# Kernel tuning notes

Hardware: AMD Instinct MI355X
Metric: run time of the kernel (lower is better)

## Reference

```python
import jax, jax.numpy as jnp
import numpy as np

B, S, D = 2, 2048, 4096
H, KV, HD = 32, 8, 128          # query heads, kv heads, head_dim
N_REP = H // KV                 # GQA groups = 4
ROPE_THETA = 1000000.0


def setup_inputs() -> dict:
    key = jax.random.key(0)
    ks = jax.random.split(key, 8)
    s = 0.02
    return {
        "hidden_states": jax.random.normal(ks[0], (B, S, D), jnp.float32),
        "position_ids": jnp.broadcast_to(jnp.arange(S, dtype=jnp.int32)[None, :], (B, S)),
        "wq": jax.random.normal(ks[1], (D, H * HD), jnp.float32) * s,
        "bq": jax.random.normal(ks[2], (H * HD,), jnp.float32) * s,
        "wk": jax.random.normal(ks[3], (D, KV * HD), jnp.float32) * s,
        "bk": jax.random.normal(ks[4], (KV * HD,), jnp.float32) * s,
        "wv": jax.random.normal(ks[5], (D, KV * HD), jnp.float32) * s,
        "bv": jax.random.normal(ks[6], (KV * HD,), jnp.float32) * s,
        "wo": jax.random.normal(ks[7], (H * HD, D), jnp.float32) * s,
    }


def _rope_cos_sin(position_ids, head_dim, theta):
    pos = position_ids.astype(jnp.float32)
    dim = head_dim // 2
    freqs = 1.0 / theta ** (jnp.arange(0, dim, dtype=jnp.float32) / dim)
    t = pos[..., None] * freqs[None, None, :]          # [B,S,dim]
    return jnp.cos(t)[..., None, :], jnp.sin(t)[..., None, :]  # [B,S,1,dim]


def _apply_rope(x, cos, sin):
    half = x.shape[-1] // 2
    x1, x2 = x[..., :half], x[..., half:]
    return jnp.concatenate([x1 * cos - x2 * sin, x1 * sin + x2 * cos], axis=-1)


def reference(hidden_states, position_ids, wq, bq, wk, bk, wv, bv, wo):
    q = (hidden_states @ wq + bq).reshape(B, S, H, HD)
    k = (hidden_states @ wk + bk).reshape(B, S, KV, HD)
    v = (hidden_states @ wv + bv).reshape(B, S, KV, HD)

    cos, sin = _rope_cos_sin(position_ids, HD, ROPE_THETA)
    q = _apply_rope(q, cos, sin)
    k = _apply_rope(k, cos, sin)

    # GQA: physically expand KV heads (adjacent repeats, matches repeat_kv)
    k = jnp.repeat(k, N_REP, axis=2)   # [B,S,H,HD]
    v = jnp.repeat(v, N_REP, axis=2)

    # causal bias (attention_mask defaults to all-ones, so only causal matters)
    neg = jnp.finfo(jnp.float32).min
    causal = jnp.tril(jnp.ones((S, S), dtype=bool))
    bias = jnp.where(causal, 0.0, neg).astype(jnp.float32)  # [S,S]

    scale = 1.0 / jnp.sqrt(jnp.float32(HD))
    scores = jnp.einsum("bqhd,bkhd->bhqk", q * scale, k) + bias[None, None]
    attn = jax.nn.softmax(scores, axis=-1)                  # [B,H,S,S]
    out = jnp.einsum("bhqk,bkhd->bqhd", attn, v)
    out = out.reshape(B, S, H * HD)
    return out @ wo
```

## Files before the change

kernel.cpp:

```cpp
#include <hip/hip_runtime.h>
#include <hip/hip_bf16.h>
#include <math.h>


typedef __bf16 bf16;
typedef __attribute__((ext_vector_type(8))) __bf16 bf16x8;
typedef __attribute__((ext_vector_type(4))) float f32x4;

__device__ __forceinline__ void glds16(const void* g, void* l) {
    __builtin_amdgcn_global_load_lds(
        (const __attribute__((address_space(1))) void*)g,
        (__attribute__((address_space(3))) void*)l, 16, 0, 0);
}

__device__ __forceinline__ unsigned cvt_pk_bf16(float lo, float hi) {
    unsigned r;
    asm("v_cvt_pk_bf16_f32 %0, %1, %2" : "=v"(r) : "v"(lo), "v"(hi));
    return r;
}

__global__ __launch_bounds__(256) void convert_kernel(
    const float* __restrict__ in, bf16* __restrict__ out)
{
    const size_t i0 = ((size_t)blockIdx.x * 256 + threadIdx.x) * 8;
    const float4 a = *(const float4*)(in + i0);
    const float4 b = *(const float4*)(in + i0 + 4);
    bf16x8 p;
    p[0] = (bf16)a.x; p[1] = (bf16)a.y; p[2] = (bf16)a.z; p[3] = (bf16)a.w;
    p[4] = (bf16)b.x; p[5] = (bf16)b.y; p[6] = (bf16)b.z; p[7] = (bf16)b.w;
    *(bf16x8*)(out + i0) = p;
}

__global__ __launch_bounds__(256) void transpose_conv_kernel(
    const float* __restrict__ in, bf16* __restrict__ out, int N)
{
    __shared__ bf16 tile[32 * 68];
    const int n0 = blockIdx.x * 32, k0 = blockIdx.y * 64;
    const int t = threadIdx.x;
    const int nn = t & 31, kk0 = (t >> 5) * 8;
#pragma unroll
    for (int j = 0; j < 8; ++j)
        tile[nn * 68 + kk0 + j] = (bf16)in[(size_t)(k0 + kk0 + j) * N + n0 + nn];
    __syncthreads();
    const int n2 = t >> 3, c = (t & 7) * 8;
    *(bf16x8*)(out + (size_t)(n0 + n2) * 4096 + k0 + c) = *(const bf16x8*)(&tile[n2 * 68 + c]);
}

template <int EPI, int AF32>
__global__ __launch_bounds__(256) void gemm_kernel(
    const float* __restrict__ A_f32, const bf16* __restrict__ A_bf16,
    const bf16* __restrict__ BqT, const bf16* __restrict__ BkT, const bf16* __restrict__ BvT,
    const float* __restrict__ b_q, const float* __restrict__ b_k, const float* __restrict__ b_v,
    bf16* __restrict__ q_out, bf16* __restrict__ kv_k, bf16* __restrict__ kv_v,
    float* __restrict__ f_out)
{
    constexpr int LDA = AF32 ? 34 : 32;
    __shared__ bf16 As[128 * LDA];
    __shared__ bf16 Bs[128 * 32];

    const int nt = blockIdx.x, mt = blockIdx.y;
    const int tid = threadIdx.x;
    const int wave = tid >> 6, lane = tid & 63;
    const int l15 = lane & 15, quad = lane >> 4;
    const int wm = (wave >> 1) * 64, wn = (wave & 1) * 64;

    const bf16* BT;
    const float* bias = nullptr;
    int sel = 0, ncol0;
    if (EPI == 0) {
        if (nt < 32)      { BT = BqT; bias = b_q; sel = 0; ncol0 = nt * 128; }
        else if (nt < 40) { BT = BkT; bias = b_k; sel = 1; ncol0 = (nt - 32) * 128; }
        else              { BT = BvT; bias = b_v; sel = 2; ncol0 = (nt - 40) * 128; }
    } else {
        BT = BqT; ncol0 = nt * 128;
    }
    const int row0 = mt * 128;

    const f32x4 vzero = {0.f, 0.f, 0.f, 0.f};
    f32x4 acc[4][4];
#pragma unroll
    for (int mi = 0; mi < 4; ++mi)
#pragma unroll
        for (int ni = 0; ni < 4; ++ni) acc[mi][ni] = vzero;

    const int a_row = tid >> 1, a_seg = (tid & 1) * 16;
    const int g_row = lane >> 2, g_seg = (lane & 3) * 8;

    for (int k0 = 0; k0 < 4096; k0 += 32) {
        if (AF32) {
            const float4* src = (const float4*)(A_f32 + (size_t)(row0 + a_row) * 4096 + k0 + a_seg);
            float4 f0 = src[0], f1 = src[1], f2 = src[2], f3 = src[3];
            bf16x8 p0, p1;
            p0[0] = (bf16)f0.x; p0[1] = (bf16)f0.y; p0[2] = (bf16)f0.z; p0[3] = (bf16)f0.w;
            p0[4] = (bf16)f1.x; p0[5] = (bf16)f1.y; p0[6] = (bf16)f1.z; p0[7] = (bf16)f1.w;
            p1[0] = (bf16)f2.x; p1[1] = (bf16)f2.y; p1[2] = (bf16)f2.z; p1[3] = (bf16)f2.w;
            p1[4] = (bf16)f3.x; p1[5] = (bf16)f3.y; p1[6] = (bf16)f3.z; p1[7] = (bf16)f3.w;
            *(bf16x8*)(&As[a_row * LDA + a_seg]) = p0;
            *(bf16x8*)(&As[a_row * LDA + a_seg + 8]) = p1;
        } else {
#pragma unroll
            for (int c = 0; c < 2; ++c)
                glds16(A_bf16 + (size_t)(row0 + wave * 32 + c * 16 + g_row) * 4096 + k0 + g_seg,
                       &As[(wave * 32 + c * 16) * 32]);
        }
#pragma unroll
        for (int c = 0; c < 2; ++c)
            glds16(BT + (size_t)(ncol0 + wave * 32 + c * 16 + g_row) * 4096 + k0 + g_seg,
                   &Bs[(wave * 32 + c * 16) * 32]);
        __syncthreads();

        bf16x8 af[4], bfv[4];
#pragma unroll
        for (int mi = 0; mi < 4; ++mi)
            af[mi] = *(const bf16x8*)(&As[(wm + mi * 16 + l15) * LDA + quad * 8]);
#pragma unroll
        for (int ni = 0; ni < 4; ++ni)
            bfv[ni] = *(const bf16x8*)(&Bs[(wn + ni * 16 + l15) * 32 + quad * 8]);
#pragma unroll
        for (int mi = 0; mi < 4; ++mi)
#pragma unroll
            for (int ni = 0; ni < 4; ++ni)
                acc[mi][ni] = __builtin_amdgcn_mfma_f32_16x16x32_bf16(af[mi], bfv[ni], acc[mi][ni], 0, 0, 0);
        __syncthreads();
    }

#pragma unroll
    for (int mi = 0; mi < 4; ++mi)
#pragma unroll
        for (int ni = 0; ni < 4; ++ni)
#pragma unroll
            for (int i = 0; i < 4; ++i) {
                const int gr = row0 + wm + mi * 16 + quad * 4 + i;
                const int gc = ncol0 + wn + ni * 16 + l15;
                float vv = acc[mi][ni][i];
                if (EPI == 1) {
                    f_out[(size_t)gr * 4096 + gc] = vv;
                } else {
                    vv += bias[gc];
                    if (sel == 0) {
                        q_out[(size_t)gr * 4096 + gc] = (bf16)vv;
                    } else {
                        bf16* dst = (sel == 1) ? kv_k : kv_v;
                        dst[(size_t)((gr >> 11) * 8 + (gc >> 7)) * 262144 +
                            (size_t)(gr & 2047) * 128 + (gc & 127)] = (bf16)vv;
                    }
                }
            }
}

__global__ __launch_bounds__(256) void rope_q_kernel(
    bf16* __restrict__ q, const int* __restrict__ pos_ids)
{
    const int idx = blockIdx.x * 256 + threadIdx.x;
    const int d = idx & 63, h = (idx >> 6) & 31, tok = idx >> 11;
    const float posv = (float)pos_ids[tok];
    const float fr = exp2f((float)d * (-19.931568569324174f / 64.f));
    float sn, cs;
    sincosf(posv * fr, &sn, &cs);
    bf16* xp = q + (size_t)tok * 4096 + h * 128 + d;
    const float x1 = (float)xp[0], x2 = (float)xp[64];
    const float scale = 0.08838834764831845f;
    xp[0]  = (bf16)((x1 * cs - x2 * sn) * scale);
    xp[64] = (bf16)((x1 * sn + x2 * cs) * scale);
}

__global__ __launch_bounds__(256) void rope_k_kernel(
    bf16* __restrict__ k, const int* __restrict__ pos_ids)
{
    const int idx = blockIdx.x * 256 + threadIdx.x;
    const int d = idx & 63, s = (idx >> 6) & 2047, bk = idx >> 17;
    const int b = bk >> 3;
    const float posv = (float)pos_ids[b * 2048 + s];
    const float fr = exp2f((float)d * (-19.931568569324174f / 64.f));
    float sn, cs;
    sincosf(posv * fr, &sn, &cs);
    bf16* xp = k + ((size_t)bk * 2048 + s) * 128 + d;
    const float x1 = (float)xp[0], x2 = (float)xp[64];
    xp[0]  = (bf16)(x1 * cs - x2 * sn);
    xp[64] = (bf16)(x1 * sn + x2 * cs);
}

__global__ __launch_bounds__(256) void attn_kernel(
    const bf16* __restrict__ q, const bf16* __restrict__ k,
    const bf16* __restrict__ v, bf16* __restrict__ o)
{
    __shared__ bf16 Ksl[64 * 136];
    __shared__ bf16 Vsl[128 * 72];
    __shared__ bf16 Psl[4 * 16 * 68];

    const int pair = blockIdx.x & 7;
    const int h  = (blockIdx.x >> 3) & 31;
    const int b  = blockIdx.x >> 8;
    const int kvh = h >> 2;
    const int tid = threadIdx.x;
    const int wave = tid >> 6, lane = tid & 63;
    const int l15 = lane & 15, quad = lane >> 4;

    const bf16* kbase = k + (size_t)(b * 8 + kvh) * 2048 * 128;
    const bf16* vbase = v + (size_t)(b * 8 + kvh) * 2048 * 128;

    const int kr = tid >> 2, ksg = (tid & 3) * 32;
    const f32x4 vzero = {0.f, 0.f, 0.f, 0.f};

#pragma unroll 1
    for (int phase = 0; phase < 2; ++phase) {
        const int qt = phase ? (15 - pair) : pair;
        const int qbase = qt * 128 + wave * 32;

        bf16x8 qf[2][4];
#pragma unroll
        for (int mi = 0; mi < 2; ++mi) {
            const bf16* qrow = q + ((size_t)(b * 2048 + qbase + mi * 16 + l15) * 32 + h) * 128;
#pragma unroll
            for (int kb = 0; kb < 4; ++kb)
                qf[mi][kb] = *(const bf16x8*)(qrow + kb * 32 + quad * 8);
        }

        f32x4 acc_o[2][8];
#pragma unroll
        for (int mi = 0; mi < 2; ++mi)
#pragma unroll
            for (int i = 0; i < 8; ++i) acc_o[mi][i] = vzero;
        float m_i[2] = {-INFINITY, -INFINITY};
        float l_i[2] = {0.f, 0.f};

        const int nT = 2 * qt + 2;
        for (int t = 0; t < nT; ++t) {
            const int kv0 = t * 64;
            {
                const bf16x8* ks = (const bf16x8*)(kbase + (size_t)(kv0 + kr) * 128 + ksg);
                bf16x8* kd = (bf16x8*)(&Ksl[kr * 136 + ksg]);
                kd[0] = ks[0]; kd[1] = ks[1]; kd[2] = ks[2]; kd[3] = ks[3];
            }
            {
                const bf16x8* vs = (const bf16x8*)(vbase + (size_t)(kv0 + lane) * 128 + wave * 32);
                bf16x8 w0 = vs[0], w1 = vs[1], w2 = vs[2], w3 = vs[3];
#pragma unroll
                for (int i = 0; i < 8; ++i) {
                    Vsl[(wave * 32 + i)      * 72 + lane] = w0[i];
                    Vsl[(wave * 32 + 8 + i)  * 72 + lane] = w1[i];
                    Vsl[(wave * 32 + 16 + i) * 72 + lane] = w2[i];
                    Vsl[(wave * 32 + 24 + i) * 72 + lane] = w3[i];
                }
            }
            __syncthreads();

            if (kv0 <= qbase + 31) {
                f32x4 sacc[2][4];
#pragma unroll
                for (int mi = 0; mi < 2; ++mi)
#pragma unroll
                    for (int nt = 0; nt < 4; ++nt) sacc[mi][nt] = vzero;
                __builtin_amdgcn_s_setprio(1);
#pragma unroll
                for (int nt = 0; nt < 4; ++nt)
#pragma unroll
                    for (int kb = 0; kb < 4; ++kb) {
                        const bf16x8 kf = *(const bf16x8*)(&Ksl[(nt * 16 + l15) * 136 + kb * 32 + quad * 8]);
                        sacc[0][nt] = __builtin_amdgcn_mfma_f32_16x16x32_bf16(kf, qf[0][kb], sacc[0][nt], 0, 0, 0);
                        sacc[1][nt] = __builtin_amdgcn_mfma_f32_16x16x32_bf16(kf, qf[1][kb], sacc[1][nt], 0, 0, 0);
                    }
                __builtin_amdgcn_s_setprio(0);

                bf16x8 pf[2][2];
#pragma unroll
                for (int mi = 0; mi < 2; ++mi) {
                    const int rb = qbase + mi * 16;
                    if (kv0 + 63 > rb) {
#pragma unroll
                        for (int nt = 0; nt < 4; ++nt) {
                            const int kvr = kv0 + nt * 16 + quad * 4;
#pragma unroll
                            for (int i = 0; i < 4; ++i)
                                if (kvr + i > rb + l15) sacc[mi][nt][i] = -INFINITY;
                        }
                    }
                    float tm;
                    {
                        f32x4 m4;
#pragma unroll
                        for (int i = 0; i < 4; ++i)
                            m4[i] = fmaxf(fmaxf(sacc[mi][0][i], sacc[mi][1][i]),
                                          fmaxf(sacc[mi][2][i], sacc[mi][3][i]));
                        tm = fmaxf(fmaxf(m4[0], m4[1]), fmaxf(m4[2], m4[3]));
                        tm = fmaxf(tm, __shfl_xor(tm, 16, 64));
                        tm = fmaxf(tm, __shfl_xor(tm, 32, 64));
                    }
                    if (!__all(tm - m_i[mi] <= 8.f)) {
                        const float mnew = fmaxf(m_i[mi], tm);
                        const float alpha = __expf(m_i[mi] - mnew);
                        m_i[mi] = mnew;
                        l_i[mi] *= alpha;
                        float aw[4];
#pragma unroll
                        for (int i = 0; i < 4; ++i)
                            aw[i] = __shfl(alpha, quad * 4 + i, 16);
#pragma unroll
                        for (int dn = 0; dn < 8; ++dn)
#pragma unroll
                            for (int i = 0; i < 4; ++i) acc_o[mi][dn][i] *= aw[i];
                    }
                    float p[4][4];
                    float rs = 0.f;
#pragma unroll
                    for (int nt = 0; nt < 4; ++nt)
#pragma unroll
                        for (int i = 0; i < 4; ++i) {
                            p[nt][i] = __expf(sacc[mi][nt][i] - m_i[mi]);
                            rs += p[nt][i];
                        }
                    rs += __shfl_xor(rs, 16, 64);
                    rs += __shfl_xor(rs, 32, 64);
                    l_i[mi] += rs;
#pragma unroll
                    for (int nt = 0; nt < 4; ++nt) {
                        uint2 w;
                        w.x = cvt_pk_bf16(p[nt][0], p[nt][1]);
                        w.y = cvt_pk_bf16(p[nt][2], p[nt][3]);
                        *(uint2*)(&Psl[wave * 1088 + l15 * 68 + nt * 16 + quad * 4]) = w;
                    }
#pragma unroll
                    for (int k2 = 0; k2 < 2; ++k2)
                        pf[mi][k2] = *(const bf16x8*)(&Psl[wave * 1088 + l15 * 68 + k2 * 32 + quad * 8]);
                }

                __builtin_amdgcn_s_setprio(1);
#pragma unroll
                for (int dn = 0; dn < 8; ++dn)
#pragma unroll
                    for (int k2 = 0; k2 < 2; ++k2) {
                        const bf16x8 vf = *(const bf16x8*)(&Vsl[(dn * 16 + l15) * 72 + k2 * 32 + quad * 8]);
                        acc_o[0][dn] = __builtin_amdgcn_mfma_f32_16x16x32_bf16(pf[0][k2], vf, acc_o[0][dn], 0, 0, 0);
                        acc_o[1][dn] = __builtin_amdgcn_mfma_f32_16x16x32_bf16(pf[1][k2], vf, acc_o[1][dn], 0, 0, 0);
                    }
                __builtin_amdgcn_s_setprio(0);
            }
            __syncthreads();
        }

#pragma unroll
        for (int mi = 0; mi < 2; ++mi) {
            const float inv = 1.f / l_i[mi];
            float invw[4];
#pragma unroll
            for (int i = 0; i < 4; ++i)
                invw[i] = __shfl(inv, quad * 4 + i, 16);
#pragma unroll
            for (int dn = 0; dn < 8; ++dn)
#pragma unroll
                for (int i = 0; i < 4; ++i) {
                    const int s = qbase + mi * 16 + quad * 4 + i;
                    o[(((size_t)b * 2048 + s) * 32 + h) * 128 + dn * 16 + l15] =
                        (bf16)(acc_o[mi][dn][i] * invw[i]);
                }
        }
    }
}

extern "C" void kernel_launch(void* const* d_in, const int* in_sizes, int n_in,
                              void* d_out, int out_size, void* d_ws, size_t ws_size,
                              hipStream_t stream)
{
    (void)in_sizes; (void)n_in; (void)out_size;
    const float* hidden = (const float*)d_in[0];
    const int*   pos    = (const int*)d_in[1];
    const float* wq     = (const float*)d_in[2];
    const float* bq_    = (const float*)d_in[3];
    const float* wk     = (const float*)d_in[4];
    const float* bk_    = (const float*)d_in[5];
    const float* wv     = (const float*)d_in[6];
    const float* bv_    = (const float*)d_in[7];
    const float* wo     = (const float*)d_in[8];
    float* out = (float*)d_out;

    char* ws = (char*)d_ws;
    bf16* wqT   = (bf16*)(ws);
    bf16* wkT   = (bf16*)(ws + 33554432);
    bf16* wvT   = (bf16*)(ws + 41943040);
    bf16* q_pre = (bf16*)(ws + 50331648);
    bf16* k_t   = (bf16*)(ws + 83886080);
    bf16* v_t   = (bf16*)(ws + 92274688);
    bf16* hid_b = (bf16*)(ws + 100663296);
    bf16* attn_o = wqT;
    bf16* woT    = q_pre;
    const bool have_hid = (ws_size >= 134217728);

    transpose_conv_kernel<<<dim3(128, 64), 256, 0, stream>>>(wq, wqT, 4096);
    transpose_conv_kernel<<<dim3(32, 64), 256, 0, stream>>>(wk, wkT, 1024);
    transpose_conv_kernel<<<dim3(32, 64), 256, 0, stream>>>(wv, wvT, 1024);

    if (have_hid) {
        convert_kernel<<<8192, 256, 0, stream>>>(hidden, hid_b);
        gemm_kernel<0, 0><<<dim3(48, 32), 256, 0, stream>>>(
            nullptr, hid_b, wqT, wkT, wvT, bq_, bk_, bv_, q_pre, k_t, v_t, nullptr);
    } else {
        gemm_kernel<0, 1><<<dim3(48, 32), 256, 0, stream>>>(
            hidden, nullptr, wqT, wkT, wvT, bq_, bk_, bv_, q_pre, k_t, v_t, nullptr);
    }

    rope_q_kernel<<<32768, 256, 0, stream>>>(q_pre, pos);
    rope_k_kernel<<<8192, 256, 0, stream>>>(k_t, pos);

    attn_kernel<<<512, 256, 0, stream>>>(q_pre, k_t, v_t, attn_o);

    transpose_conv_kernel<<<dim3(128, 64), 256, 0, stream>>>(wo, woT, 4096);

    gemm_kernel<1, 0><<<dim3(32, 32), 256, 0, stream>>>(
        nullptr, attn_o, woT, nullptr, nullptr, nullptr, nullptr, nullptr,
        nullptr, nullptr, nullptr, out);
}
```

Measured before the change: 872.5 us.

## Add 256x256-tile 8-wave pipelined GEMM for QKV and output projections

Adds a new bf16 GEMM kernel that uses 256x256 output tiles with 512 threads and 128 KB of LDS. It double-buffers K slices with global_load_lds in a staged pipeline, uses XOR-swizzled LDS layouts and s_setprio around MFMA bursts, and remaps workgroups for cache locality. The kernel replaces the 128x128 GEMM for the QKV and output projections when the workspace holds the bf16 hidden buffer. The goal is more data reuse per tile and overlap of loads with MFMA work. The cost is lower occupancy and a smaller grid (384 and 256 blocks), which may leave CUs underused.

```diff
diff --git a/kernel.cpp b/kernel.cpp
--- a/kernel.cpp
+++ b/kernel.cpp
@@ -44,6 +44,173 @@
     __syncthreads();
     const int n2 = t >> 3, c = (t & 7) * 8;
     *(bf16x8*)(out + (size_t)(n0 + n2) * 4096 + k0 + c) = *(const bf16x8*)(&tile[n2 * 68 + c]);
+}
+
+#define G256_LDA(dst, bufv, mh)                                                 \
+    do {                                                                        \
+        _Pragma("unroll")                                                       \
+        for (int m_ = 0; m_ < 4; ++m_) {                                        \
+            const int rowh_ = (m_ * 2 + wr) * 16 + l15;                         \
+            const int colp_ = (quad * 8) ^ (((rowh_ >> 3) & 1) << 4);           \
+            const int bse_ = ((bufv) * 2 + (mh)) * 8192 + rowh_ * 32 + colp_;   \
+            dst[m_][0] = *(const bf16x8*)&Lds[bse_];                            \
+            dst[m_][1] = *(const bf16x8*)&Lds[bse_ + 4096];                     \
+        }                                                                       \
+    } while (0)
+
+#define G256_LDB(dst, bufv, nh)                                                 \
+    do {                                                                        \
+        _Pragma("unroll")                                                       \
+        for (int n_ = 0; n_ < 2; ++n_) {                                        \
+            const int rowh_ = (n_ * 4 + wc) * 16 + l15;                         \
+            const int colp_ = (quad * 8) ^ (((rowh_ >> 3) & 1) << 4);           \
+            const int bse_ = 32768 + ((bufv) * 2 + (nh)) * 8192 +               \
+                             rowh_ * 32 + colp_;                                \
+            dst[n_][0] = *(const bf16x8*)&Lds[bse_];                            \
+            dst[n_][1] = *(const bf16x8*)&Lds[bse_ + 4096];                     \
+        }                                                                       \
+    } while (0)
+
+#define G256_QUAD(av, bv, mh, nh)                                               \
+    do {                                                                        \
+        __builtin_amdgcn_s_setprio(1);                                          \
+        _Pragma("unroll")                                                       \
+        for (int m_ = 0; m_ < 4; ++m_)                                          \
+            _Pragma("unroll")                                                   \
+            for (int n_ = 0; n_ < 2; ++n_) {                                    \
+                acc[(mh) * 4 + m_][(nh) * 2 + n_] =                             \
+                    __builtin_amdgcn_mfma_f32_16x16x32_bf16(                    \
+                        av[m_][0], bv[n_][0], acc[(mh) * 4 + m_][(nh) * 2 + n_],\
+                        0, 0, 0);                                               \
+                acc[(mh) * 4 + m_][(nh) * 2 + n_] =                             \
+                    __builtin_amdgcn_mfma_f32_16x16x32_bf16(                    \
+                        av[m_][1], bv[n_][1], acc[(mh) * 4 + m_][(nh) * 2 + n_],\
+                        0, 0, 0);                                               \
+            }                                                                   \
+        __builtin_amdgcn_s_setprio(0);                                          \
+    } while (0)
+
+template <int EPI>
+__global__ __launch_bounds__(512) void gemm256_kernel(
+    const bf16* __restrict__ A,
+    const bf16* __restrict__ BqT, const bf16* __restrict__ BkT, const bf16* __restrict__ BvT,
+    const float* __restrict__ b_q, const float* __restrict__ b_k, const float* __restrict__ b_v,
+    bf16* __restrict__ q_out, bf16* __restrict__ kv_k, bf16* __restrict__ kv_v,
+    float* __restrict__ f_out, int nwg)
+{
+    __shared__ bf16 Lds[65536];
+
+    const int tid = threadIdx.x;
+    const int wv = tid >> 6, lane = tid & 63;
+    const int l15 = lane & 15, quad = lane >> 4;
+    const int wr = wv >> 2, wc = wv & 3;
+
+    const int bid = blockIdx.x;
+    const int swz = (bid & 7) * (nwg >> 3) + (bid >> 3);
+    const int mt = swz & 15, nt = swz >> 4;
+    const int row0 = mt * 256;
+
+    const bf16* BT;
+    const float* biasp = nullptr;
+    bf16* dstkv = nullptr;
+    int sel = 0, bcol0, ocol0 = nt * 256, lcol0 = 0;
+    if (EPI == 0) {
+        if (nt < 16)      { BT = BqT; bcol0 = nt * 256; biasp = b_q + nt * 256; sel = 0; }
+        else if (nt < 20) { BT = BkT; bcol0 = (nt - 16) * 256; biasp = b_k + (nt - 16) * 256;
+                            sel = 1; dstkv = kv_k; lcol0 = (nt - 16) * 256; }
+        else              { BT = BvT; bcol0 = (nt - 20) * 256; biasp = b_v + (nt - 20) * 256;
+                            sel = 2; dstkv = kv_v; lcol0 = (nt - 20) * 256; }
+    } else {
+        BT = BqT; bcol0 = nt * 256;
+    }
+
+    auto stage = [&](int n) {
+        if (n >= 256) return;
+        const int T = n >> 2, j = n & 3;
+        const int buf = T & 1;
+        const bool isA = (j == 0 || j == 3);
+        const int half = (j == 0) ? 0 : (j == 3) ? 1 : (j - 1);
+        const int k0 = T * 64;
+        const bf16* g = isA ? (A + (size_t)(row0 + half * 128) * 4096)
+                            : (BT + (size_t)(bcol0 + half * 128) * 4096);
+        bf16* lb = &Lds[(isA ? 0 : 32768) + (buf * 2 + half) * 8192];
+#pragma unroll
+        for (int jj = 0; jj < 2; ++jj) {
+            const int pc = (wv * 2 + jj) * 64 + lane;
+            const int kk = pc >> 9, rem = pc & 511;
+            const int row = rem >> 2, ccp = rem & 3;
+            const int ccl = ccp ^ ((row >> 2) & 2);
+            glds16(g + (size_t)row * 4096 + k0 + kk * 32 + ccl * 8,
+                   lb + (wv * 2 + jj) * 512);
+        }
+    };
+
+    const f32x4 vzero = {0.f, 0.f, 0.f, 0.f};
+    f32x4 acc[8][4];
+#pragma unroll
+    for (int mi = 0; mi < 8; ++mi)
+#pragma unroll
+        for (int ni = 0; ni < 4; ++ni) acc[mi][ni] = vzero;
+
+    bf16x8 a[4][2], b0[2][2], b1[2][2];
+
+    for (int n = 0; n < 7; ++n) stage(n);
+    asm volatile("s_waitcnt vmcnt(6)" ::: "memory");
+    __builtin_amdgcn_s_barrier();
+
+    for (int t = 0; t < 64; ++t) {
+        const int buf = t & 1;
+        const int nb = 4 * t;
+        G256_LDA(a, buf, 0);
+        G256_LDB(b0, buf, 0);
+        stage(nb + 7);
+        __builtin_amdgcn_s_barrier();
+        G256_QUAD(a, b0, 0, 0);
+        __builtin_amdgcn_s_barrier();
+        G256_LDB(b1, buf, 1);
+        stage(nb + 8);
+        __builtin_amdgcn_s_barrier();
+        G256_QUAD(a, b1, 0, 1);
+        __builtin_amdgcn_s_barrier();
+        G256_LDA(a, buf, 1);
+        stage(nb + 9);
+        __builtin_amdgcn_s_barrier();
+        G256_QUAD(a, b0, 1, 0);
+        __builtin_amdgcn_s_barrier();
+        stage(nb + 10);
+        __builtin_amdgcn_s_barrier();
+        G256_QUAD(a, b1, 1, 1);
+        if (t < 62)       asm volatile("s_waitcnt vmcnt(6)" ::: "memory");
+        else if (t == 62) asm volatile("s_waitcnt vmcnt(0)" ::: "memory");
+        __builtin_amdgcn_s_barrier();
+    }
+
+#pragma unroll
+    for (int mi = 0; mi < 8; ++mi) {
+        const int mtile = (mi >> 2) * 8 + (mi & 3) * 2 + wr;
+#pragma unroll
+        for (int ni = 0; ni < 4; ++ni) {
+            const int ntile = ni * 4 + wc;
+            const int gcl = ntile * 16 + l15;
+#pragma unroll
+            for (int i = 0; i < 4; ++i) {
+                const int gr = row0 + mtile * 16 + quad * 4 + i;
+                float vv = acc[mi][ni][i];
+                if (EPI == 1) {
+                    f_out[(size_t)gr * 4096 + ocol0 + gcl] = vv;
+                } else {
+                    vv += biasp[gcl];
+                    if (sel == 0) {
+                        q_out[(size_t)gr * 4096 + ocol0 + gcl] = (bf16)vv;
+                    } else {
+                        const int lc = lcol0 + gcl;
+                        dstkv[(size_t)((gr >> 11) * 8 + (lc >> 7)) * 262144 +
+                              (size_t)(gr & 2047) * 128 + (lc & 127)] = (bf16)vv;
+                    }
+                }
+            }
+        }
+    }
 }
 
 template <int EPI, int AF32>
@@ -391,8 +558,8 @@
 
     if (have_hid) {
         convert_kernel<<<8192, 256, 0, stream>>>(hidden, hid_b);
-        gemm_kernel<0, 0><<<dim3(48, 32), 256, 0, stream>>>(
-            nullptr, hid_b, wqT, wkT, wvT, bq_, bk_, bv_, q_pre, k_t, v_t, nullptr);
+        gemm256_kernel<0><<<384, 512, 0, stream>>>(
+            hid_b, wqT, wkT, wvT, bq_, bk_, bv_, q_pre, k_t, v_t, nullptr, 384);
     } else {
         gemm_kernel<0, 1><<<dim3(48, 32), 256, 0, stream>>>(
             hidden, nullptr, wqT, wkT, wvT, bq_, bk_, bv_, q_pre, k_t, v_t, nullptr);
@@ -405,7 +572,13 @@
 
     transpose_conv_kernel<<<dim3(128, 64), 256, 0, stream>>>(wo, woT, 4096);
 
-    gemm_kernel<1, 0><<<dim3(32, 32), 256, 0, stream>>>(
-        nullptr, attn_o, woT, nullptr, nullptr, nullptr, nullptr, nullptr,
-        nullptr, nullptr, nullptr, out);
-}
+    if (have_hid) {
+        gemm256_kernel<1><<<256, 512, 0, stream>>>(
+            attn_o, woT, nullptr, nullptr, nullptr, nullptr, nullptr,
+            nullptr, nullptr, nullptr, out, 256);
+    } else {
+        gemm_kernel<1, 0><<<dim3(32, 32), 256, 0, stream>>>(
+            nullptr, attn_o, woT, nullptr, nullptr, nullptr, nullptr, nullptr,
+            nullptr, nullptr, nullptr, out);
+    }
+}
```

Measured after the change: 796.7 us. 8.7% less time.
